# Performance work log

Measured on AMD Instinct MI355X. Metric: run time of the kernel, lower is better.

## Reference

```python
import jax, jax.numpy as jnp
import numpy as np

B, N, C_IN, C_OUT, HID = 2, 512, 16, 16, 64


def setup_inputs() -> dict:
    key = jax.random.key(0)
    ks = jax.random.split(key, 6)
    return {
        "features": jax.random.normal(ks[0], (B, N, C_IN), dtype=jnp.float32),
        "geometry": jax.random.normal(ks[1], (B, N, 3), dtype=jnp.float32),
        "W1": jax.random.normal(ks[2], (HID, 4), dtype=jnp.float32) * 0.5,
        "b1": jax.random.normal(ks[3], (HID,), dtype=jnp.float32) * 0.1,
        "W2": jax.random.normal(ks[4], (C_OUT * C_IN, HID), dtype=jnp.float32) * 0.1,
        "b2": jax.random.normal(ks[5], (C_OUT * C_IN,), dtype=jnp.float32) * 0.1,
    }


def reference(features, geometry, W1, b1, W2, b2):
    # rb = geometry.unsqueeze(1) -> [z,1,b,xyz]; ra = geometry.unsqueeze(2) -> [z,a,1,xyz]
    rel = geometry[:, None, :, :] - geometry[:, :, None, :]  # [z, a, b, 3] = rb - ra
    # kernel network: MLP on (rel, |rel|) -> [z, a, b, C_out, C_in]
    r2 = jnp.sum(rel * rel, axis=-1, keepdims=True)
    norm = jnp.sqrt(r2 + 1e-12)                              # differentiable at 0
    feat = jnp.concatenate([rel, norm], axis=-1)             # [z, a, b, 4]
    h = jax.nn.gelu(jnp.einsum('zabf,hf->zabh', feat, W1) + b1)
    k = (jnp.einsum('zabh,oh->zabo', h, W2) + b2)            # [z, a, b, C_out*C_in]
    z, a, b = k.shape[:3]
    k = k.reshape(z, a, b, C_OUT, C_IN)
    # contraction: torch.einsum('zabij,zbj->zabi')
    return jnp.einsum('zabij,zbj->zabi', k, features)
```

## Files before the change

kernel.cpp:

```cpp
#include <hip/hip_runtime.h>

#define NQ   512
#define CI   16
#define CO   16
#define HIDN 64

typedef __attribute__((ext_vector_type(8))) short bf16x8;
typedef __attribute__((ext_vector_type(4))) float f32x4;

__device__ __forceinline__ unsigned cvt_pk_bf16(float a, float b) {
    unsigned r;
    asm("v_cvt_pk_bf16_f32 %0, %1, %2" : "=v"(r) : "v"(a), "v"(b));
    return r;
}

__global__ __launch_bounds__(512) void fused_mfma_kernel(
    const float* __restrict__ features,
    const float* __restrict__ geometry,
    const float* __restrict__ W1,
    const float* __restrict__ b1,
    const float* __restrict__ W2,
    const float* __restrict__ b2,
    float* __restrict__ out)
{
    __shared__ float M_sm[CO][68];
    __shared__ float c_sm[CO];

    const int zb  = blockIdx.x;
    const int z   = zb >> 9;
    const int b   = zb & 511;
    const int tid = threadIdx.x;

    float f[CI];
    #pragma unroll
    for (int j = 0; j < CI; ++j) f[j] = features[zb * CI + j];

    #pragma unroll
    for (int e = 0; e < 2; ++e) {
        int idx = tid + e * 512;
        int i = idx >> 6, k = idx & 63;
        float acc = 0.f;
        #pragma unroll
        for (int j = 0; j < CI; ++j)
            acc = fmaf(f[j], W2[(i * CI + j) * HIDN + k], acc);
        M_sm[i][k] = acc;
    }
    if (tid < CO) {
        float acc = 0.f;
        #pragma unroll
        for (int j = 0; j < CI; ++j)
            acc = fmaf(f[j], b2[tid * CI + j], acc);
        c_sm[tid] = acc;
    }
    __syncthreads();

    const int wv   = tid >> 6;
    const int lane = tid & 63;
    const int col  = lane & 15;
    const int g    = lane >> 4;

    bf16x8 Bf[2][2];
    #pragma unroll
    for (int kc = 0; kc < 2; ++kc) {
        const float* mp = &M_sm[col][kc * 32 + g * 8];
        unsigned hpk[4], lpk[4];
        #pragma unroll
        for (int p = 0; p < 4; ++p) {
            float m0 = mp[2 * p], m1 = mp[2 * p + 1];
            unsigned h = cvt_pk_bf16(m0, m1);
            float h0 = __builtin_bit_cast(float, h << 16);
            float h1 = __builtin_bit_cast(float, h & 0xffff0000u);
            hpk[p] = h;
            lpk[p] = cvt_pk_bf16(m0 - h0, m1 - h1);
        }
        union { unsigned u[4]; bf16x8 v; } uh, ul;
        #pragma unroll
        for (int p = 0; p < 4; ++p) { uh.u[p] = hpk[p]; ul.u[p] = lpk[p]; }
        Bf[0][kc] = uh.v;
        Bf[1][kc] = ul.v;
    }

    const float gbx = geometry[(z * NQ + b) * 3 + 0];
    const float gby = geometry[(z * NQ + b) * 3 + 1];
    const float gbz = geometry[(z * NQ + b) * 3 + 2];
    const int abase = wv * 64;

    float rel[4][4];
    #pragma unroll
    for (int t = 0; t < 4; ++t) {
        const float* ga = geometry + (size_t)(z * NQ + abase + t * 16 + col) * 3;
        float rx = gbx - ga[0], ry = gby - ga[1], rz = gbz - ga[2];
        rel[t][0] = rx; rel[t][1] = ry; rel[t][2] = rz;
        rel[t][3] = sqrtf(fmaf(rx, rx, fmaf(ry, ry, rz * rz)) + 1e-12f);
    }

    const float cinit = c_sm[col];
    f32x4 acc[4];
    #pragma unroll
    for (int t = 0; t < 4; ++t) acc[t] = (f32x4){cinit, cinit, cinit, cinit};

    #pragma unroll
    for (int kc = 0; kc < 2; ++kc) {
        float4 w[8]; float bb[8];
        #pragma unroll
        for (int j = 0; j < 8; ++j) {
            int h = kc * 32 + g * 8 + j;
            w[j]  = *reinterpret_cast<const float4*>(W1 + h * 4);
            bb[j] = b1[h];
        }
        #pragma unroll
        for (int t = 0; t < 4; ++t) {
            float hv[8];
            #pragma unroll
            for (int j = 0; j < 8; ++j) {
                float x = bb[j];
                x = fmaf(rel[t][0], w[j].x, x);
                x = fmaf(rel[t][1], w[j].y, x);
                x = fmaf(rel[t][2], w[j].z, x);
                x = fmaf(rel[t][3], w[j].w, x);
                float q = fmaf(x * x, 0.044715f, 1.0f);
                float e = __builtin_amdgcn_exp2f((-2.3022082f * x) * q);
                hv[j]   = x * __builtin_amdgcn_rcpf(1.0f + e);
            }
            union { unsigned u[4]; bf16x8 v; } ua;
            #pragma unroll
            for (int p = 0; p < 4; ++p)
                ua.u[p] = cvt_pk_bf16(hv[2 * p], hv[2 * p + 1]);
            acc[t] = __builtin_amdgcn_mfma_f32_16x16x32_bf16(ua.v, Bf[0][kc], acc[t], 0, 0, 0);
            acc[t] = __builtin_amdgcn_mfma_f32_16x16x32_bf16(ua.v, Bf[1][kc], acc[t], 0, 0, 0);
        }
    }

    #pragma unroll
    for (int t = 0; t < 4; ++t) {
        #pragma unroll
        for (int r = 0; r < 4; ++r) {
            int arow = abase + t * 16 + g * 4 + r;
            out[(((size_t)(z * NQ + arow)) * NQ + b) * CO + col] = acc[t][r];
        }
    }
}

extern "C" void kernel_launch(void* const* d_in, const int* in_sizes, int n_in,
                              void* d_out, int out_size, void* d_ws, size_t ws_size,
                              hipStream_t stream) {
    const float* features = (const float*)d_in[0];
    const float* geometry = (const float*)d_in[1];
    const float* W1       = (const float*)d_in[2];
    const float* b1       = (const float*)d_in[3];
    const float* W2       = (const float*)d_in[4];
    const float* b2       = (const float*)d_in[5];
    float* out = (float*)d_out;

    fused_mfma_kernel<<<1024, 512, 0, stream>>>(
        features, geometry, W1, b1, W2, b2, out);
}
```

Before: 25.26 us.

## Swap MFMA operands for vectorized stores, split blocks in half, vectorize W2 prep

```diff
diff --git a/kernel.cpp b/kernel.cpp
--- a/kernel.cpp
+++ b/kernel.cpp
@@ -14,7 +14,7 @@
     return r;
 }
 
-__global__ __launch_bounds__(512) void fused_mfma_kernel(
+__global__ __launch_bounds__(256, 4) void fused_mfma_kernel(
     const float* __restrict__ features,
     const float* __restrict__ geometry,
     const float* __restrict__ W1,
@@ -23,43 +23,63 @@
     const float* __restrict__ b2,
     float* __restrict__ out)
 {
-    __shared__ float M_sm[CO][68];
+    __shared__ __attribute__((aligned(16))) float M_sm[CO][68];
     __shared__ float c_sm[CO];
+    __shared__ float f_sm[CI];
 
-    const int zb  = blockIdx.x;
+    const int bid = blockIdx.x;
+    const int zb  = bid >> 1;
+    const int a0  = (bid & 1) << 8;
     const int z   = zb >> 9;
     const int b   = zb & 511;
     const int tid = threadIdx.x;
 
-    float f[CI];
-    #pragma unroll
-    for (int j = 0; j < CI; ++j) f[j] = features[zb * CI + j];
-
-    #pragma unroll
-    for (int e = 0; e < 2; ++e) {
-        int idx = tid + e * 512;
-        int i = idx >> 6, k = idx & 63;
-        float acc = 0.f;
-        #pragma unroll
-        for (int j = 0; j < CI; ++j)
-            acc = fmaf(f[j], W2[(i * CI + j) * HIDN + k], acc);
-        M_sm[i][k] = acc;
-    }
-    if (tid < CO) {
-        float acc = 0.f;
-        #pragma unroll
-        for (int j = 0; j < CI; ++j)
-            acc = fmaf(f[j], b2[tid * CI + j], acc);
-        c_sm[tid] = acc;
-    }
+    if (tid < CI) f_sm[tid] = features[zb * CI + tid];
     __syncthreads();
 
     const int wv   = tid >> 6;
     const int lane = tid & 63;
     const int col  = lane & 15;
     const int g    = lane >> 4;
+    const int abase = a0 + wv * 64;
 
-    bf16x8 Bf[2][2];
+    const float gbx = geometry[(z * NQ + b) * 3 + 0];
+    const float gby = geometry[(z * NQ + b) * 3 + 1];
+    const float gbz = geometry[(z * NQ + b) * 3 + 2];
+    float rel[4][4];
+    #pragma unroll
+    for (int t = 0; t < 4; ++t) {
+        const float* ga = geometry + (size_t)(z * NQ + abase + t * 16 + col) * 3;
+        float rx = gbx - ga[0], ry = gby - ga[1], rz = gbz - ga[2];
+        rel[t][0] = rx; rel[t][1] = ry; rel[t][2] = rz;
+        rel[t][3] = sqrtf(fmaf(rx, rx, fmaf(ry, ry, rz * rz)) + 1e-12f);
+    }
+
+    {
+        const int i  = tid >> 4;
+        const int k4 = (tid & 15) * 4;
+        float4 acc = {0.f, 0.f, 0.f, 0.f};
+        #pragma unroll
+        for (int j = 0; j < CI; ++j) {
+            const float fj = f_sm[j];
+            const float4 w2 = *reinterpret_cast<const float4*>(&W2[(i * CI + j) * HIDN + k4]);
+            acc.x = fmaf(fj, w2.x, acc.x);
+            acc.y = fmaf(fj, w2.y, acc.y);
+            acc.z = fmaf(fj, w2.z, acc.z);
+            acc.w = fmaf(fj, w2.w, acc.w);
+        }
+        *reinterpret_cast<float4*>(&M_sm[i][k4]) = acc;
+    }
+    if (tid < CO) {
+        float acc = 0.f;
+        #pragma unroll
+        for (int j = 0; j < CI; ++j)
+            acc = fmaf(f_sm[j], b2[tid * CI + j], acc);
+        c_sm[tid] = acc;
+    }
+    __syncthreads();
+
+    bf16x8 Af[2][2];
     #pragma unroll
     for (int kc = 0; kc < 2; ++kc) {
         const float* mp = &M_sm[col][kc * 32 + g * 8];
@@ -76,28 +96,16 @@
         union { unsigned u[4]; bf16x8 v; } uh, ul;
         #pragma unroll
         for (int p = 0; p < 4; ++p) { uh.u[p] = hpk[p]; ul.u[p] = lpk[p]; }
-        Bf[0][kc] = uh.v;
-        Bf[1][kc] = ul.v;
+        Af[0][kc] = uh.v;
+        Af[1][kc] = ul.v;
     }
 
-    const float gbx = geometry[(z * NQ + b) * 3 + 0];
-    const float gby = geometry[(z * NQ + b) * 3 + 1];
-    const float gbz = geometry[(z * NQ + b) * 3 + 2];
-    const int abase = wv * 64;
-
-    float rel[4][4];
+    f32x4 cin;
     #pragma unroll
-    for (int t = 0; t < 4; ++t) {
-        const float* ga = geometry + (size_t)(z * NQ + abase + t * 16 + col) * 3;
-        float rx = gbx - ga[0], ry = gby - ga[1], rz = gbz - ga[2];
-        rel[t][0] = rx; rel[t][1] = ry; rel[t][2] = rz;
-        rel[t][3] = sqrtf(fmaf(rx, rx, fmaf(ry, ry, rz * rz)) + 1e-12f);
-    }
-
-    const float cinit = c_sm[col];
+    for (int r = 0; r < 4; ++r) cin[r] = c_sm[g * 4 + r];
     f32x4 acc[4];
     #pragma unroll
-    for (int t = 0; t < 4; ++t) acc[t] = (f32x4){cinit, cinit, cinit, cinit};
+    for (int t = 0; t < 4; ++t) acc[t] = cin;
 
     #pragma unroll
     for (int kc = 0; kc < 2; ++kc) {
@@ -126,18 +134,15 @@
             #pragma unroll
             for (int p = 0; p < 4; ++p)
                 ua.u[p] = cvt_pk_bf16(hv[2 * p], hv[2 * p + 1]);
-            acc[t] = __builtin_amdgcn_mfma_f32_16x16x32_bf16(ua.v, Bf[0][kc], acc[t], 0, 0, 0);
-            acc[t] = __builtin_amdgcn_mfma_f32_16x16x32_bf16(ua.v, Bf[1][kc], acc[t], 0, 0, 0);
+            acc[t] = __builtin_amdgcn_mfma_f32_16x16x32_bf16(Af[0][kc], ua.v, acc[t], 0, 0, 0);
+            acc[t] = __builtin_amdgcn_mfma_f32_16x16x32_bf16(Af[1][kc], ua.v, acc[t], 0, 0, 0);
         }
     }
 
     #pragma unroll
     for (int t = 0; t < 4; ++t) {
-        #pragma unroll
-        for (int r = 0; r < 4; ++r) {
-            int arow = abase + t * 16 + g * 4 + r;
-            out[(((size_t)(z * NQ + arow)) * NQ + b) * CO + col] = acc[t][r];
-        }
+        float* op = out + (((size_t)(z * NQ + abase + t * 16 + col)) * NQ + b) * CO + g * 4;
+        *reinterpret_cast<f32x4*>(op) = acc[t];
     }
 }
 
@@ -152,6 +157,6 @@
     const float* b2       = (const float*)d_in[5];
     float* out = (float*)d_out;
 
-    fused_mfma_kernel<<<1024, 512, 0, stream>>>(
+    fused_mfma_kernel<<<2048, 256, 0, stream>>>(
         features, geometry, W1, b1, W2, b2, out);
 }
```

After: 26.74 us. 5.9% more time.
